# Performance work log

Measured on AMD Instinct MI355X. Metric: run time of the kernel, lower is better.

The kernel has to match this reference:

```python
import jax, jax.numpy as jnp
import numpy as np

NUM_HEADS = 16
EMBED_DIM = 2048
MAX_SEQ = 2048
HEAD_SIZE = EMBED_DIM // NUM_HEADS  # 128
ROPE_BASE = 10000.0


def setup_inputs() -> dict:
    key = jax.random.key(0)
    k1, k2, k3 = jax.random.split(key, 3)
    B, S = 4, 2048
    x = jax.random.normal(k1, (B, S, EMBED_DIM), dtype=jnp.float32)
    positions = jnp.arange(S, dtype=jnp.int32)
    # causal boolean mask: query i may attend to key j iff j <= i
    mask = jnp.tril(jnp.ones((S, MAX_SEQ), dtype=bool))[None, None]
    Wqkv = jax.random.normal(k2, (EMBED_DIM, 3 * EMBED_DIM), dtype=jnp.float32) * 0.02
    Wout = jax.random.normal(k3, (EMBED_DIM, EMBED_DIM), dtype=jnp.float32) * 0.02
    return {"x": x, "positions": positions, "mask": mask, "Wqkv": Wqkv, "Wout": Wout}


def _rope(x, positions):
    # x: [B, S, H, hd]; rotate interleaved (even, odd) pairs in last dim
    inv_freq = 1.0 / (ROPE_BASE ** (jnp.arange(0, HEAD_SIZE, 2, dtype=jnp.float32) / HEAD_SIZE))
    freq = positions.astype(jnp.float32)[:, None] * inv_freq[None, :]  # [S, hd/2]
    cos = jnp.cos(freq)[None, :, None, :]  # [1, S, 1, hd/2]
    sin = jnp.sin(freq)[None, :, None, :]
    xp = x.reshape(*x.shape[:-1], HEAD_SIZE // 2, 2)
    x0, x1 = xp[..., 0], xp[..., 1]
    out = jnp.stack([x0 * cos - x1 * sin, x1 * cos + x0 * sin], axis=-1)
    return out.reshape(x.shape)


def reference(x, positions, mask, Wqkv, Wout):
    B, S, D = x.shape
    H, hd = NUM_HEADS, HEAD_SIZE
    qkv = x @ Wqkv  # [B, S, 3D]
    q, k, v = jnp.split(qkv, 3, axis=-1)
    q = q.reshape(B, S, H, hd)
    k = k.reshape(B, S, H, hd)
    v = v.reshape(B, S, H, hd)
    q = _rope(q, positions)
    k = _rope(k, positions)
    # [B, H, S, hd]
    q = q.transpose(0, 2, 1, 3)
    k = k.transpose(0, 2, 1, 3)
    v = v.transpose(0, 2, 1, 3)
    # KV-cache update: write k/v at `positions` into a zero-initialized cache
    cache_k = jnp.zeros((B, H, MAX_SEQ, hd), dtype=x.dtype)
    cache_v = jnp.zeros((B, H, MAX_SEQ, hd), dtype=x.dtype)
    k = cache_k.at[:, :, positions].set(k)
    v = cache_v.at[:, :, positions].set(v)
    scale = 1.0 / jnp.sqrt(jnp.float32(hd))
    scores = jnp.einsum('bhqd,bhkd->bhqk', q, k) * scale  # [B, H, S, MAX_SEQ]
    scores = jnp.where(mask, scores, jnp.float32(-1e30))
    attn = jax.nn.softmax(scores, axis=-1)
    y = jnp.einsum('bhqk,bhkd->bhqd', attn, v)  # [B, H, S, hd]
    y = y.transpose(0, 2, 1, 3).reshape(B, S, D)
    return y @ Wout
```

## Files before the change

### kernel.cpp

```cpp
#include <hip/hip_runtime.h>
#include <hip/hip_bf16.h>
#include <cstdint>
#include <cstddef>

constexpr int CS = 2048;
constexpr int CHD = 128;
constexpr int CD = 2048;
constexpr int CN3 = 6144;

typedef __attribute__((ext_vector_type(8))) short short8;
typedef __attribute__((ext_vector_type(4))) float f32x4;
typedef __attribute__((ext_vector_type(4))) int int4v;

#define GLOAD_LDS16(g, l) __builtin_amdgcn_global_load_lds( \
    (const __attribute__((address_space(1))) void*)(g),      \
    (__attribute__((address_space(3))) void*)(l), 16, 0, 0)

__device__ __forceinline__ unsigned short f2bf(float f) {
  union { float f; unsigned u; } v; v.f = f;
  unsigned r = v.u + 0x7fffu + ((v.u >> 16) & 1u);
  return (unsigned short)(r >> 16);
}
__device__ __forceinline__ unsigned pkbf(float a, float b) {
  return (unsigned)f2bf(a) | ((unsigned)f2bf(b) << 16);
}

__device__ __forceinline__ float dpp_xor1(float x) {
  return __builtin_bit_cast(float, __builtin_amdgcn_update_dpp(
      __builtin_bit_cast(int, x), __builtin_bit_cast(int, x), 0xB1, 0xf, 0xf, true));
}

__global__ __launch_bounds__(256) void k_cvt(const float* __restrict__ in,
                                             unsigned short* __restrict__ out, int n) {
  int i = (blockIdx.x * 256 + threadIdx.x) * 8;
  if (i >= n) return;
  float4 a = *(const float4*)(in + i);
  float4 b = *(const float4*)(in + i + 4);
  short8 o;
  o[0] = (short)f2bf(a.x); o[1] = (short)f2bf(a.y);
  o[2] = (short)f2bf(a.z); o[3] = (short)f2bf(a.w);
  o[4] = (short)f2bf(b.x); o[5] = (short)f2bf(b.y);
  o[6] = (short)f2bf(b.z); o[7] = (short)f2bf(b.w);
  *(short8*)(out + i) = o;
}

__global__ __launch_bounds__(256) void k_transcvt(const float* __restrict__ in,
                                                  unsigned short* __restrict__ out,
                                                  int R, int C) {
  __shared__ float tile[32][33];
  int c0 = blockIdx.x * 32, r0 = blockIdx.y * 32;
  int tx = threadIdx.x & 31, ty = threadIdx.x >> 5;
#pragma unroll
  for (int j = 0; j < 4; ++j)
    tile[ty + 8 * j][tx] = in[(size_t)(r0 + ty + 8 * j) * C + c0 + tx];
  __syncthreads();
#pragma unroll
  for (int j = 0; j < 4; ++j)
    out[(size_t)(c0 + ty + 8 * j) * R + r0 + tx] = f2bf(tile[tx][ty + 8 * j]);
}

__global__ void k_ropetab(float2* __restrict__ tab) {
  int p = blockIdx.x, c = threadIdx.x;
  float inv = powf(10000.0f, -(float)(2 * c) / 128.0f);
  float a = (float)p * inv;
  tab[p * 64 + c] = make_float2(cosf(a), sinf(a));
}

template <int EPI>
__global__ __launch_bounds__(512, 2) void k_gemm256(
    const unsigned short* __restrict__ A,
    const unsigned short* __restrict__ Bt,
    float* __restrict__ outF,
    unsigned short* __restrict__ outQ,
    unsigned short* __restrict__ outK,
    unsigned short* __restrict__ outV,
    const int* __restrict__ positions,
    const float2* __restrict__ tab,
    int M, int N, int K, int nbn) {
  const int nwg = gridDim.x;
  const int cpx = nwg >> 3;
  const int wg = blockIdx.x;
  const int swz = (wg & 7) * cpx + (wg >> 3);
  const int bn = swz % nbn, bm = swz / nbn;

  const int t = threadIdx.x;
  const int w = t >> 6, lane = t & 63;
  const int wr = w >> 2, wc = w & 3;
  const int lr = lane & 15, lg = lane >> 4;

  __shared__ char L[131072];

  const size_t Kb = (size_t)K * 2;
  const int srl = w * 16 + (lane >> 3);
  const int sch = ((lane & 7) ^ (lane >> 3)) * 16;
  const char* gA = (const char*)A + (size_t)(bm * 256 + srl) * Kb + sch;
  const char* gB = (const char*)Bt + (size_t)(bn * 256 + srl) * Kb + sch;
  const int ldst = w * 2048 + lane * 16;

#define STAGE(BUFB, OP, HALF, J, KT)                                               \
  GLOAD_LDS16(((OP) ? gB : gA) + (size_t)((HALF) * 128 + (J) * 8) * Kb +           \
                  (size_t)(KT) * 128,                                              \
              L + (BUFB) + (OP) * 32768 + (HALF) * 16384 + (J) * 1024 + ldst)

  const int xo = lr & 7;
  const int aRow = (wr * 128 + lr) * 128;
  const int bRow = (wc * 64 + lr) * 128;
#define RDA(BUFB, MI, KH) \
  (*(const short8*)(L + (BUFB) + aRow + (MI) * 2048 + ((((KH) * 4 + lg) ^ xo) << 4)))
#define RDB(BUFB, NI, KH) \
  (*(const short8*)(L + (BUFB) + 32768 + bRow + (NI) * 2048 + ((((KH) * 4 + lg) ^ xo) << 4)))

  f32x4 acc[8][4] = {};
  const int ktiles = K >> 6;

#pragma unroll
  for (int h = 0; h < 2; ++h)
#pragma unroll
    for (int j = 0; j < 2; ++j) { STAGE(0, 0, h, j, 0); STAGE(0, 1, h, j, 0); }
  if (ktiles > 1) {
    STAGE(65536, 0, 0, 0, 1); STAGE(65536, 0, 0, 1, 1);
    asm volatile("s_waitcnt vmcnt(2)" ::: "memory");
  } else {
    asm volatile("s_waitcnt vmcnt(0)" ::: "memory");
  }
  __builtin_amdgcn_s_barrier();

  short8 afr[4][2], bfr[4][2];

#define KTILE_PHASES(CB, NB, KT, DOSTAGE)                                          \
                                              \
  _Pragma("unroll") for (int mi = 0; mi < 4; ++mi)                                 \
      _Pragma("unroll") for (int kh = 0; kh < 2; ++kh)                             \
          afr[mi][kh] = RDA(CB, mi, kh);                                           \
  _Pragma("unroll") for (int ni = 0; ni < 2; ++ni)                                 \
      _Pragma("unroll") for (int kh = 0; kh < 2; ++kh)                             \
          bfr[ni][kh] = RDB(CB, ni, kh);                                           \
  if (DOSTAGE) { STAGE(NB, 0, 1, 0, (KT) + 1); STAGE(NB, 0, 1, 1, (KT) + 1); }     \
  __builtin_amdgcn_s_setprio(1);                                                   \
  _Pragma("unroll") for (int mi = 0; mi < 4; ++mi)                                 \
      _Pragma("unroll") for (int ni = 0; ni < 2; ++ni)                             \
          _Pragma("unroll") for (int kh = 0; kh < 2; ++kh)                         \
              acc[mi][ni] = __builtin_amdgcn_mfma_f32_16x16x32_bf16(               \
                  afr[mi][kh], bfr[ni][kh], acc[mi][ni], 0, 0, 0);                 \
  __builtin_amdgcn_s_setprio(0);                                                   \
                                                     \
  _Pragma("unroll") for (int ni = 2; ni < 4; ++ni)                                 \
      _Pragma("unroll") for (int kh = 0; kh < 2; ++kh)                             \
          bfr[ni][kh] = RDB(CB, ni, kh);                                           \
  if (DOSTAGE) { STAGE(NB, 1, 0, 0, (KT) + 1); STAGE(NB, 1, 0, 1, (KT) + 1); }     \
  __builtin_amdgcn_s_setprio(1);                                                   \
  _Pragma("unroll") for (int mi = 0; mi < 4; ++mi)                                 \
      _Pragma("unroll") for (int ni = 2; ni < 4; ++ni)                             \
          _Pragma("unroll") for (int kh = 0; kh < 2; ++kh)                         \
              acc[mi][ni] = __builtin_amdgcn_mfma_f32_16x16x32_bf16(               \
                  afr[mi][kh], bfr[ni][kh], acc[mi][ni], 0, 0, 0);                 \
  __builtin_amdgcn_s_setprio(0);                                                   \
                                                    \
  _Pragma("unroll") for (int mi = 0; mi < 4; ++mi)                                 \
      _Pragma("unroll") for (int kh = 0; kh < 2; ++kh)                             \
          afr[mi][kh] = RDA(CB, mi + 4, kh);                                       \
  if (DOSTAGE) { STAGE(NB, 1, 1, 0, (KT) + 1); STAGE(NB, 1, 1, 1, (KT) + 1); }     \
  __builtin_amdgcn_s_setprio(1);                                                   \
  _Pragma("unroll") for (int mi = 0; mi < 4; ++mi)                                 \
      _Pragma("unroll") for (int ni = 2; ni < 4; ++ni)                             \
          _Pragma("unroll") for (int kh = 0; kh < 2; ++kh)                         \
              acc[mi + 4][ni] = __builtin_amdgcn_mfma_f32_16x16x32_bf16(           \
                  afr[mi][kh], bfr[ni][kh], acc[mi + 4][ni], 0, 0, 0);             \
  __builtin_amdgcn_s_setprio(0);                                                   \
                                                       \
  __builtin_amdgcn_s_setprio(1);                                                   \
  _Pragma("unroll") for (int mi = 0; mi < 4; ++mi)                                 \
      _Pragma("unroll") for (int ni = 0; ni < 2; ++ni)                             \
          _Pragma("unroll") for (int kh = 0; kh < 2; ++kh)                         \
              acc[mi + 4][ni] = __builtin_amdgcn_mfma_f32_16x16x32_bf16(           \
                  afr[mi][kh], bfr[ni][kh], acc[mi + 4][ni], 0, 0, 0);             \
  __builtin_amdgcn_s_setprio(0);

  int c = 0;
  for (int kt = 0; kt < ktiles - 1; ++kt) {
    const int cb = c << 16, nb = (c ^ 1) << 16;
    KTILE_PHASES(cb, nb, kt, true)
    __builtin_amdgcn_s_barrier();
    if (kt + 2 < ktiles) {
      STAGE(cb, 0, 0, 0, kt + 2); STAGE(cb, 0, 0, 1, kt + 2);
      asm volatile("s_waitcnt vmcnt(2)" ::: "memory");
    } else {
      asm volatile("s_waitcnt vmcnt(0)" ::: "memory");
    }
    __builtin_amdgcn_s_barrier();
    c ^= 1;
  }
  {
    const int cb = c << 16, nb = 0;
    KTILE_PHASES(cb, nb, 0, false)
  }
#undef KTILE_PHASES
#undef STAGE
#undef RDA
#undef RDB

  if constexpr (EPI == 0) {
    const int which = bn >> 3;
    if (which < 2) {
      const float qsc = which ? 1.0f : 0.08838834764831845f;
      unsigned short* dstB = which ? outK : outQ;
#pragma unroll
      for (int mi = 0; mi < 8; ++mi)
#pragma unroll
        for (int rr = 0; rr < 4; ++rr) {
          int mg = bm * 256 + wr * 128 + mi * 16 + lg * 4 + rr;
          int bb = mg >> 11, s = mg & 2047;
          int pos = positions[s];
          int srow2 = which ? pos : s;
          const float2* tb = tab + pos * 64 + wc * 32 + (lr >> 1);
#pragma unroll
          for (int ni = 0; ni < 4; ++ni) {
            int cn = bn * 256 + wc * 64 + ni * 16 + lr;
            int h = (cn >> 7) & 15, d = cn & 127;
            float x = acc[mi][ni][rr];
            float p = dpp_xor1(x);
            float2 cs = tb[ni * 8];
            float y = (lr & 1) ? (x * cs.x + p * cs.y)
                               : (x * cs.x - p * cs.y);
            dstB[((size_t)(bb * 16 + h) * CS + srow2) * CHD + d] = f2bf(y * qsc);
          }
        }
    } else {
      __syncthreads();
      unsigned short* TL = (unsigned short*)L;
#pragma unroll
      for (int mi = 0; mi < 8; ++mi) {
        int sb = wr * 128 + mi * 16 + lg * 4;
#pragma unroll
        for (int ni = 0; ni < 4; ++ni) {
          int vc = wc * 64 + ni * 16 + lr;
          unsigned lo = pkbf(acc[mi][ni][0], acc[mi][ni][1]);
          unsigned hi2 = pkbf(acc[mi][ni][2], acc[mi][ni][3]);
          unsigned long long v8 = (unsigned long long)lo | ((unsigned long long)hi2 << 32);
          *(unsigned long long*)(TL + vc * 256 + (sb ^ ((vc & 7) << 3))) = v8;
        }
      }
      __syncthreads();
      const int row = t >> 1, half = t & 1;
      const int bb = bm >> 3, s0 = (bm & 7) * 256;
      const int h0 = bn * 2 - 32;
      unsigned short* vrow = outV +
          ((size_t)((bb * 16 + h0 + (row >> 7)) * 128 + (row & 127))) * CS + s0 + half * 128;
#pragma unroll
      for (int j = 0; j < 16; ++j) {
        short8 v = *(const short8*)(TL + row * 256 + ((half * 128 + j * 8) ^ ((row & 7) << 3)));
        *(short8*)(vrow + j * 8) = v;
      }
    }
  } else {
#pragma unroll
    for (int mi = 0; mi < 8; ++mi)
#pragma unroll
      for (int rr = 0; rr < 4; ++rr) {
        int mg = bm * 256 + wr * 128 + mi * 16 + lg * 4 + rr;
#pragma unroll
        for (int ni = 0; ni < 4; ++ni)
          outF[(size_t)mg * N + bn * 256 + wc * 64 + ni * 16 + lr] = acc[mi][ni][rr];
      }
  }
}

__global__ __launch_bounds__(256, 3) void k_attn(
    const unsigned short* __restrict__ Q,
    const unsigned short* __restrict__ Kc,
    const unsigned short* __restrict__ Vt,
    unsigned short* __restrict__ Y) {
  const int qt_h = 15 - (blockIdx.x >> 6);
  const int bh = blockIdx.x & 63;
  const int q0 = qt_h * 128;
  const int t = threadIdx.x;
  const int w = t >> 6, lane = t & 63;
  const int lr = lane & 15, lg = lane >> 4;
  const int b = bh >> 4, h = bh & 15;

  __shared__ unsigned short lK[3][32 * 128];
  __shared__ unsigned short lVt[3][128 * 32];

  const char* kg = (const char*)(Kc + (size_t)bh * CS * CHD);
  const char* vtg = (const char*)(Vt + (size_t)bh * CHD * CS);

  short8 qf[2][4];
#pragma unroll
  for (int qt = 0; qt < 2; ++qt)
#pragma unroll
    for (int ks = 0; ks < 4; ++ks)
      qf[qt][ks] = *(const short8*)(Q + ((size_t)bh * CS + q0 + w * 32 + qt * 16 + lr) * CHD + ks * 32 + lg * 8);

  f32x4 accy[2][8] = {};
  f32x4 accl[2] = {};
  float m[2] = {-1e30f, -1e30f};

  short8 vone;
  {
    short o16 = (lr == 0) ? (short)0x3F80 : (short)0;
#pragma unroll
    for (int e = 0; e < 8; ++e) vone[e] = o16;
  }

  const int nch = 4 * qt_h + 4;
  const int qmaxw = q0 + w * 32 + 31;

  auto stage = [&](int ch, int buf) {
    const int kv0 = ch * 32;
    char* dK = (char*)lK[buf];
    char* dV = (char*)lVt[buf];
#pragma unroll
    for (int i = 0; i < 2; ++i) {
      int kr = w * 8 + i * 4 + lg;
      GLOAD_LDS16(kg + (size_t)(kv0 + kr) * 256 + ((lr * 16) ^ ((kr & 7) << 4)),
                  dK + w * 2048 + i * 1024 + lane * 16);
    }
#pragma unroll
    for (int i = 0; i < 2; ++i) {
      int vd = w * 32 + i * 16 + (lane >> 2);
      GLOAD_LDS16(vtg + (size_t)vd * 4096 + (size_t)kv0 * 2 + (lane & 3) * 16,
                  dV + w * 2048 + i * 1024 + lane * 16);
    }
  };

  stage(0, 0);
  stage(1, 1);
  int cur = 0, nxt = 2;
  for (int ch = 0; ch < nch; ++ch) {
    if (ch + 1 < nch) {
      asm volatile("s_waitcnt vmcnt(4)" ::: "memory");
    } else {
      asm volatile("s_waitcnt vmcnt(0)" ::: "memory");
    }
    __builtin_amdgcn_s_barrier();
    if (ch + 2 < nch) stage(ch + 2, nxt);

    const int kv0 = ch * 32;
    const unsigned short* bK = lK[cur];
    const unsigned short* bV = lVt[cur];
    cur = cur == 2 ? 0 : cur + 1;
    nxt = nxt == 2 ? 0 : nxt + 1;

    if (kv0 <= qmaxw) {
      f32x4 sv[2][2] = {};
#pragma unroll
      for (int kvt = 0; kvt < 2; ++kvt) {
        short8 kf[4];
#pragma unroll
        for (int ks = 0; ks < 4; ++ks) {
          int row = kvt * 16 + lr;
          kf[ks] = *(const short8*)((const char*)bK + row * 256 + ((ks * 64 + lg * 16) ^ ((row & 7) << 4)));
        }
#pragma unroll
        for (int qt = 0; qt < 2; ++qt)
#pragma unroll
          for (int ks = 0; ks < 4; ++ks)
            sv[qt][kvt] = __builtin_amdgcn_mfma_f32_16x16x32_bf16(kf[ks], qf[qt][ks], sv[qt][kvt], 0, 0, 0);
      }

      float p8[2][8];
      float pm[2];
      bool need = false;
#pragma unroll
      for (int qt = 0; qt < 2; ++qt) {
        const int qi = q0 + w * 32 + qt * 16 + lr;
        float mx = -1e30f;
#pragma unroll
        for (int kvt = 0; kvt < 2; ++kvt)
#pragma unroll
          for (int r = 0; r < 4; ++r) {
            int kv = kv0 + kvt * 16 + lg * 4 + r;
            float s = (kv <= qi) ? sv[qt][kvt][r] : -1e30f;
            p8[qt][kvt * 4 + r] = s;
            mx = fmaxf(mx, s);
          }
        mx = fmaxf(mx, __shfl_xor(mx, 32, 64));
        mx = fmaxf(mx, __shfl_xor(mx, 16, 64));
        pm[qt] = mx;
        need = need || (mx > m[qt] + 8.0f);
      }

      if (__any((int)need)) {
#pragma unroll
        for (int qt = 0; qt < 2; ++qt) {
          float nm = fmaxf(m[qt], pm[qt]);
          float fr = __expf(m[qt] - nm);
          m[qt] = nm;
#pragma unroll
          for (int r = 0; r < 4; ++r) {
            int idx = (((lane >> 4) << 2) + r) << 2;
            float frT = __builtin_bit_cast(float,
                __builtin_amdgcn_ds_bpermute(idx, __builtin_bit_cast(int, fr)));
#pragma unroll
            for (int dt = 0; dt < 8; ++dt) accy[qt][dt][r] *= frT;
            accl[qt][r] *= frT;
          }
        }
      }

      short8 pa[2];
      const int sA = lr + ((lane & 16) << 1);
      const int sB = sA + 16;
      const bool hi = (lane >= 32);
#pragma unroll
      for (int qt = 0; qt < 2; ++qt) {
        float pe0 = __expf(p8[qt][0] - m[qt]);
        float pe1 = __expf(p8[qt][1] - m[qt]);
        float pe2 = __expf(p8[qt][2] - m[qt]);
        float pe3 = __expf(p8[qt][3] - m[qt]);
        float pe4 = __expf(p8[qt][4] - m[qt]);
        float pe5 = __expf(p8[qt][5] - m[qt]);
        float pe6 = __expf(p8[qt][6] - m[qt]);
        float pe7 = __expf(p8[qt][7] - m[qt]);
        unsigned w0 = pkbf(pe0, pe1);
        unsigned w1 = pkbf(pe2, pe3);
        unsigned w2 = pkbf(pe4, pe5);
        unsigned w3 = pkbf(pe6, pe7);
        unsigned a0 = (unsigned)__shfl((int)w0, sA, 64);
        unsigned a2 = (unsigned)__shfl((int)w2, sA, 64);
        unsigned b0 = (unsigned)__shfl((int)w1, sA, 64);
        unsigned b2 = (unsigned)__shfl((int)w3, sA, 64);
        unsigned c0 = (unsigned)__shfl((int)w0, sB, 64);
        unsigned c2 = (unsigned)__shfl((int)w2, sB, 64);
        unsigned d0 = (unsigned)__shfl((int)w1, sB, 64);
        unsigned d2 = (unsigned)__shfl((int)w3, sB, 64);
        int4v xi;
        xi[0] = (int)(hi ? a2 : a0);
        xi[1] = (int)(hi ? b2 : b0);
        xi[2] = (int)(hi ? c2 : c0);
        xi[3] = (int)(hi ? d2 : d0);
        pa[qt] = __builtin_bit_cast(short8, xi);
      }

#pragma unroll
      for (int dt = 0; dt < 8; ++dt) {
        short8 vf = *(const short8*)((const char*)bV + (dt * 16 + lr) * 64 + lg * 16);
#pragma unroll
        for (int qt = 0; qt < 2; ++qt)
          accy[qt][dt] = __builtin_amdgcn_mfma_f32_16x16x32_bf16(pa[qt], vf, accy[qt][dt], 0, 0, 0);
      }
#pragma unroll
      for (int qt = 0; qt < 2; ++qt)
        accl[qt] = __builtin_amdgcn_mfma_f32_16x16x32_bf16(pa[qt], vone, accl[qt], 0, 0, 0);
    }
  }

#pragma unroll
  for (int qt = 0; qt < 2; ++qt)
#pragma unroll
    for (int r = 0; r < 4; ++r) {
      float lsum = accl[qt][r];
      lsum = __shfl(lsum, lane & 48, 64);
      float inv = 1.0f / lsum;
      int qrow = q0 + w * 32 + qt * 16 + lg * 4 + r;
      unsigned short* yr = Y + ((size_t)(b * CS + qrow)) * CD + h * CHD;
#pragma unroll
      for (int dt = 0; dt < 8; ++dt)
        yr[dt * 16 + lr] = f2bf(accy[qt][dt][r] * inv);
    }
}

extern "C" void kernel_launch(void* const* d_in, const int* in_sizes, int n_in,
                              void* d_out, int out_size, void* d_ws, size_t ws_size,
                              hipStream_t stream) {
  const float* x = (const float*)d_in[0];
  const int* positions = (const int*)d_in[1];
  const float* Wqkv = (const float*)d_in[3];
  const float* Wout = (const float*)d_in[4];
  float* out = (float*)d_out;

  char* ws = (char*)d_ws;
  size_t off = 0;
  auto alloc = [&](size_t bytes) {
    char* p = ws + off;
    off += (bytes + 255) & ~(size_t)255;
    return p;
  };
  unsigned short* q_bf = (unsigned short*)alloc((size_t)64 * CS * CHD * 2);
  unsigned short* k_bf = (unsigned short*)alloc((size_t)64 * CS * CHD * 2);
  unsigned short* v_bf = (unsigned short*)alloc((size_t)64 * CS * CHD * 2);
  unsigned short* xw = (unsigned short*)alloc((size_t)8192 * CD * 2);
  unsigned short* wT = (unsigned short*)alloc((size_t)CN3 * CD * 2);
  float2* tab = (float2*)alloc((size_t)CS * 64 * sizeof(float2));


  k_cvt<<<8192, 256, 0, stream>>>(x, xw, 8192 * CD);
  k_transcvt<<<dim3(CN3 / 32, CD / 32), 256, 0, stream>>>(Wqkv, wT, CD, CN3);
  k_ropetab<<<CS, 64, 0, stream>>>(tab);
  k_gemm256<0><<<768, 512, 0, stream>>>(xw, wT, nullptr, q_bf, k_bf, v_bf,
                                        positions, tab, 8192, CN3, CD, 24);
  k_transcvt<<<dim3(CD / 32, CD / 32), 256, 0, stream>>>(Wout, wT, CD, CD);
  k_attn<<<1024, 256, 0, stream>>>(q_bf, k_bf, v_bf, xw);
  k_gemm256<1><<<256, 512, 0, stream>>>(xw, wT, out, nullptr, nullptr, nullptr,
                                        nullptr, nullptr, 8192, CD, CD, 8);
}
```

Measured before the change: 411.5 us.

## Add K=32 double-buffered QKV GEMM with 64KB LDS and split V epilogue

Adds a dedicated QKV projection GEMM that stages 32-wide K tiles in a 64KB double buffer instead of the previous 128KB layout. The MFMA phases are interleaved with the global-to-LDS loads. The V-transpose epilogue now runs in two halves, one per wave row, so it fits in the smaller LDS. The aim is lower LDS use, which could raise occupancy or latency hiding, at the cost of more barriers per K step and shorter tiles for hiding load latency.

New measurement: 424.8 us. 1.03x slower.

```diff
diff --git a/kernel.cpp b/kernel.cpp
--- a/kernel.cpp
+++ b/kernel.cpp
@@ -66,16 +66,206 @@
   tab[p * 64 + c] = make_float2(cosf(a), sinf(a));
 }
 
+__global__ __launch_bounds__(512, 2) void k_gemm32(
+    const unsigned short* __restrict__ A,
+    const unsigned short* __restrict__ Bt,
+    unsigned short* __restrict__ outQ,
+    unsigned short* __restrict__ outK,
+    unsigned short* __restrict__ outV,
+    const int* __restrict__ positions,
+    const float2* __restrict__ tab,
+    int K, int nbn) {
+  const int nwg = gridDim.x;
+  const int cpx = nwg >> 3;
+  const int wg = blockIdx.x;
+  const int swz = (wg & 7) * cpx + (wg >> 3);
+  const int bn = swz % nbn, bm = swz / nbn;
+
+  const int t = threadIdx.x;
+  const int w = t >> 6, lane = t & 63;
+  const int wr = w >> 2, wc = w & 3;
+  const int lr = lane & 15, lg = lane >> 4;
+
+  __shared__ char L[65536];
+
+  const size_t Kb = (size_t)K * 2;
+  const int srow = t >> 2;
+  const int sslot = ((t & 3) ^ ((t >> 3) & 3)) * 16;
+  const char* gA = (const char*)A + (size_t)(bm * 256 + srow) * Kb + sslot;
+  const char* gB = (const char*)Bt + (size_t)(bn * 256 + srow) * Kb + sslot;
+
+#define STG(BUFB, OP, J, KT)                                                   \
+  GLOAD_LDS16(((OP) ? gB : gA) + (size_t)((J) * 128) * Kb + (size_t)(KT) * 64, \
+              L + (BUFB) + (OP) * 16384 + (J) * 8192 + t * 16)
+
+  const int xo2 = (lr >> 1) & 3;
+  const int aR = (wr * 128 + lr) * 64;
+  const int bR = (wc * 64 + lr) * 64;
+#define RA(BUFB, MI) (*(const short8*)(L + (BUFB) + aR + (MI) * 1024 + ((lg ^ xo2) << 4)))
+#define RB(BUFB, NI) (*(const short8*)(L + (BUFB) + 16384 + bR + (NI) * 1024 + ((lg ^ xo2) << 4)))
+
+  f32x4 acc[8][4] = {};
+  const int ktiles = K >> 5;
+
+  STG(0, 0, 0, 0); STG(0, 0, 1, 0); STG(0, 1, 0, 0); STG(0, 1, 1, 0);
+  STG(32768, 0, 0, 1);
+  asm volatile("s_waitcnt vmcnt(1)" ::: "memory");
+  __builtin_amdgcn_s_barrier();
+
+  short8 af[4], bf[4];
+  int c = 0;
+  for (int kt = 0; kt < ktiles - 1; ++kt) {
+    const int cb = c << 15, nb = (c ^ 1) << 15;
+#pragma unroll
+    for (int mi = 0; mi < 4; ++mi) af[mi] = RA(cb, mi);
+#pragma unroll
+    for (int ni = 0; ni < 2; ++ni) bf[ni] = RB(cb, ni);
+    STG(nb, 0, 1, kt + 1);
+    __builtin_amdgcn_s_setprio(1);
+#pragma unroll
+    for (int mi = 0; mi < 4; ++mi)
+#pragma unroll
+      for (int ni = 0; ni < 2; ++ni)
+        acc[mi][ni] = __builtin_amdgcn_mfma_f32_16x16x32_bf16(af[mi], bf[ni], acc[mi][ni], 0, 0, 0);
+    __builtin_amdgcn_s_setprio(0);
+#pragma unroll
+    for (int ni = 2; ni < 4; ++ni) bf[ni] = RB(cb, ni);
+    STG(nb, 1, 0, kt + 1);
+    __builtin_amdgcn_s_setprio(1);
+#pragma unroll
+    for (int mi = 0; mi < 4; ++mi)
+#pragma unroll
+      for (int ni = 2; ni < 4; ++ni)
+        acc[mi][ni] = __builtin_amdgcn_mfma_f32_16x16x32_bf16(af[mi], bf[ni], acc[mi][ni], 0, 0, 0);
+    __builtin_amdgcn_s_setprio(0);
+#pragma unroll
+    for (int mi = 0; mi < 4; ++mi) af[mi] = RA(cb, mi + 4);
+    STG(nb, 1, 1, kt + 1);
+    __builtin_amdgcn_s_setprio(1);
+#pragma unroll
+    for (int mi = 0; mi < 4; ++mi)
+#pragma unroll
+      for (int ni = 2; ni < 4; ++ni)
+        acc[mi + 4][ni] = __builtin_amdgcn_mfma_f32_16x16x32_bf16(af[mi], bf[ni], acc[mi + 4][ni], 0, 0, 0);
+    __builtin_amdgcn_s_setprio(0);
+    __builtin_amdgcn_s_setprio(1);
+#pragma unroll
+    for (int mi = 0; mi < 4; ++mi)
+#pragma unroll
+      for (int ni = 0; ni < 2; ++ni)
+        acc[mi + 4][ni] = __builtin_amdgcn_mfma_f32_16x16x32_bf16(af[mi], bf[ni], acc[mi + 4][ni], 0, 0, 0);
+    __builtin_amdgcn_s_setprio(0);
+
+    __builtin_amdgcn_s_barrier();
+    if (kt + 2 < ktiles) {
+      STG(cb, 0, 0, kt + 2);
+      asm volatile("s_waitcnt vmcnt(1)" ::: "memory");
+    } else {
+      asm volatile("s_waitcnt vmcnt(0)" ::: "memory");
+    }
+    __builtin_amdgcn_s_barrier();
+    c ^= 1;
+  }
+  {
+    const int cb = c << 15;
+#pragma unroll
+    for (int mi = 0; mi < 4; ++mi) af[mi] = RA(cb, mi);
+#pragma unroll
+    for (int ni = 0; ni < 2; ++ni) bf[ni] = RB(cb, ni);
+    __builtin_amdgcn_s_setprio(1);
+#pragma unroll
+    for (int mi = 0; mi < 4; ++mi)
+#pragma unroll
+      for (int ni = 0; ni < 2; ++ni)
+        acc[mi][ni] = __builtin_amdgcn_mfma_f32_16x16x32_bf16(af[mi], bf[ni], acc[mi][ni], 0, 0, 0);
+    __builtin_amdgcn_s_setprio(0);
+#pragma unroll
+    for (int ni = 2; ni < 4; ++ni) bf[ni] = RB(cb, ni);
+    __builtin_amdgcn_s_setprio(1);
+#pragma unroll
+    for (int mi = 0; mi < 4; ++mi)
+#pragma unroll
+      for (int ni = 2; ni < 4; ++ni)
+        acc[mi][ni] = __builtin_amdgcn_mfma_f32_16x16x32_bf16(af[mi], bf[ni], acc[mi][ni], 0, 0, 0);
+    __builtin_amdgcn_s_setprio(0);
+#pragma unroll
+    for (int mi = 0; mi < 4; ++mi) af[mi] = RA(cb, mi + 4);
+    __builtin_amdgcn_s_setprio(1);
+#pragma unroll
+    for (int mi = 0; mi < 4; ++mi)
+#pragma unroll
+      for (int ni = 0; ni < 4; ++ni)
+        acc[mi + 4][ni] = __builtin_amdgcn_mfma_f32_16x16x32_bf16(af[mi], bf[ni], acc[mi + 4][ni], 0, 0, 0);
+    __builtin_amdgcn_s_setprio(0);
+  }
+#undef STG
+#undef RA
+#undef RB
+
+  const int which = bn >> 3;
+  if (which < 2) {
+    const float qsc = which ? 1.0f : 0.08838834764831845f;
+    unsigned short* dstB = which ? outK : outQ;
+#pragma unroll
+    for (int mi = 0; mi < 8; ++mi)
+#pragma unroll
+      for (int rr = 0; rr < 4; ++rr) {
+        int mg = bm * 256 + wr * 128 + mi * 16 + lg * 4 + rr;
+        int bb = mg >> 11, s = mg & 2047;
+        int pos = positions[s];
+        int srow2 = which ? pos : s;
+        const float2* tb = tab + pos * 64 + wc * 32 + (lr >> 1);
+#pragma unroll
+        for (int ni = 0; ni < 4; ++ni) {
+          int cn = bn * 256 + wc * 64 + ni * 16 + lr;
+          int h = (cn >> 7) & 15, d = cn & 127;
+          float x = acc[mi][ni][rr];
+          float p = dpp_xor1(x);
+          float2 cs = tb[ni * 8];
+          float y = (lr & 1) ? (x * cs.x + p * cs.y)
+                             : (x * cs.x - p * cs.y);
+          dstB[((size_t)(bb * 16 + h) * CS + srow2) * CHD + d] = f2bf(y * qsc);
+        }
+      }
+  } else {
+    unsigned short* TL = (unsigned short*)L;
+    const int bb = bm >> 3, s0 = (bm & 7) * 256;
+    const int h0 = bn * 2 - 32;
+    const int vcr = t >> 1, hs = t & 1;
+    unsigned short* vrow = outV +
+        ((size_t)((bb * 16 + h0 + (vcr >> 7)) * 128 + (vcr & 127))) * CS + s0;
+#pragma unroll
+    for (int hh = 0; hh < 2; ++hh) {
+      __syncthreads();
+      if (wr == hh) {
+#pragma unroll
+        for (int mi = 0; mi < 8; ++mi) {
+          int sb = mi * 16 + lg * 4;
+#pragma unroll
+          for (int ni = 0; ni < 4; ++ni) {
+            int vc = wc * 64 + ni * 16 + lr;
+            unsigned lo = pkbf(acc[mi][ni][0], acc[mi][ni][1]);
+            unsigned hi2 = pkbf(acc[mi][ni][2], acc[mi][ni][3]);
+            unsigned long long v8 = (unsigned long long)lo | ((unsigned long long)hi2 << 32);
+            *(unsigned long long*)(TL + vc * 128 + (sb ^ ((vc & 7) << 3))) = v8;
+          }
+        }
+      }
+      __syncthreads();
+#pragma unroll
+      for (int j = 0; j < 8; ++j) {
+        short8 v = *(const short8*)(TL + vcr * 128 + ((hs * 64 + j * 8) ^ ((vcr & 7) << 3)));
+        *(short8*)(vrow + hh * 128 + hs * 64 + j * 8) = v;
+      }
+    }
+  }
+}
+
 template <int EPI>
 __global__ __launch_bounds__(512, 2) void k_gemm256(
     const unsigned short* __restrict__ A,
     const unsigned short* __restrict__ Bt,
     float* __restrict__ outF,
-    unsigned short* __restrict__ outQ,
-    unsigned short* __restrict__ outK,
-    unsigned short* __restrict__ outV,
-    const int* __restrict__ positions,
-    const float2* __restrict__ tab,
     int M, int N, int K, int nbn) {
   const int nwg = gridDim.x;
   const int cpx = nwg >> 3;
@@ -199,70 +389,15 @@
 #undef RDA
 #undef RDB
 
-  if constexpr (EPI == 0) {
-    const int which = bn >> 3;
-    if (which < 2) {
-      const float qsc = which ? 1.0f : 0.08838834764831845f;
-      unsigned short* dstB = which ? outK : outQ;
-#pragma unroll
-      for (int mi = 0; mi < 8; ++mi)
-#pragma unroll
-        for (int rr = 0; rr < 4; ++rr) {
-          int mg = bm * 256 + wr * 128 + mi * 16 + lg * 4 + rr;
-          int bb = mg >> 11, s = mg & 2047;
-          int pos = positions[s];
-          int srow2 = which ? pos : s;
-          const float2* tb = tab + pos * 64 + wc * 32 + (lr >> 1);
-#pragma unroll
-          for (int ni = 0; ni < 4; ++ni) {
-            int cn = bn * 256 + wc * 64 + ni * 16 + lr;
-            int h = (cn >> 7) & 15, d = cn & 127;
-            float x = acc[mi][ni][rr];
-            float p = dpp_xor1(x);
-            float2 cs = tb[ni * 8];
-            float y = (lr & 1) ? (x * cs.x + p * cs.y)
-                               : (x * cs.x - p * cs.y);
-            dstB[((size_t)(bb * 16 + h) * CS + srow2) * CHD + d] = f2bf(y * qsc);
-          }
-        }
-    } else {
-      __syncthreads();
-      unsigned short* TL = (unsigned short*)L;
-#pragma unroll
-      for (int mi = 0; mi < 8; ++mi) {
-        int sb = wr * 128 + mi * 16 + lg * 4;
-#pragma unroll
-        for (int ni = 0; ni < 4; ++ni) {
-          int vc = wc * 64 + ni * 16 + lr;
-          unsigned lo = pkbf(acc[mi][ni][0], acc[mi][ni][1]);
-          unsigned hi2 = pkbf(acc[mi][ni][2], acc[mi][ni][3]);
-          unsigned long long v8 = (unsigned long long)lo | ((unsigned long long)hi2 << 32);
-          *(unsigned long long*)(TL + vc * 256 + (sb ^ ((vc & 7) << 3))) = v8;
-        }
-      }
-      __syncthreads();
-      const int row = t >> 1, half = t & 1;
-      const int bb = bm >> 3, s0 = (bm & 7) * 256;
-      const int h0 = bn * 2 - 32;
-      unsigned short* vrow = outV +
-          ((size_t)((bb * 16 + h0 + (row >> 7)) * 128 + (row & 127))) * CS + s0 + half * 128;
-#pragma unroll
-      for (int j = 0; j < 16; ++j) {
-        short8 v = *(const short8*)(TL + row * 256 + ((half * 128 + j * 8) ^ ((row & 7) << 3)));
-        *(short8*)(vrow + j * 8) = v;
-      }
-    }
-  } else {
-#pragma unroll
-    for (int mi = 0; mi < 8; ++mi)
-#pragma unroll
-      for (int rr = 0; rr < 4; ++rr) {
-        int mg = bm * 256 + wr * 128 + mi * 16 + lg * 4 + rr;
-#pragma unroll
-        for (int ni = 0; ni < 4; ++ni)
-          outF[(size_t)mg * N + bn * 256 + wc * 64 + ni * 16 + lr] = acc[mi][ni][rr];
-      }
-  }
+#pragma unroll
+  for (int mi = 0; mi < 8; ++mi)
+#pragma unroll
+    for (int rr = 0; rr < 4; ++rr) {
+      int mg = bm * 256 + wr * 128 + mi * 16 + lg * 4 + rr;
+#pragma unroll
+      for (int ni = 0; ni < 4; ++ni)
+        outF[(size_t)mg * N + bn * 256 + wc * 64 + ni * 16 + lr] = acc[mi][ni][rr];
+    }
 }
 
 __global__ __launch_bounds__(256, 3) void k_attn(
@@ -487,10 +622,9 @@
   k_cvt<<<8192, 256, 0, stream>>>(x, xw, 8192 * CD);
   k_transcvt<<<dim3(CN3 / 32, CD / 32), 256, 0, stream>>>(Wqkv, wT, CD, CN3);
   k_ropetab<<<CS, 64, 0, stream>>>(tab);
-  k_gemm256<0><<<768, 512, 0, stream>>>(xw, wT, nullptr, q_bf, k_bf, v_bf,
-                                        positions, tab, 8192, CN3, CD, 24);
+  k_gemm32<<<768, 512, 0, stream>>>(xw, wT, q_bf, k_bf, v_bf,
+                                    positions, tab, CD, 24);
   k_transcvt<<<dim3(CD / 32, CD / 32), 256, 0, stream>>>(Wout, wT, CD, CD);
   k_attn<<<1024, 256, 0, stream>>>(q_bf, k_bf, v_bf, xw);
-  k_gemm256<1><<<256, 512, 0, stream>>>(xw, wT, out, nullptr, nullptr, nullptr,
-                                        nullptr, nullptr, 8192, CD, CD, 8);
-}
+  k_gemm256<1><<<256, 512, 0, stream>>>(xw, wT, out, 8192, CD, CD, 8);
+}
```
